# Performance work log

Measured on AMD Instinct MI355X. Metric: run time of the kernel, lower is better.

## Reference

```python
import jax, jax.numpy as jnp
import numpy as np

EPS = 1e-5

def setup_inputs() -> dict:
    key = jax.random.key(0)
    k1, k2, k3 = jax.random.split(key, 3)
    B, T, D, K = 8, 4096, 256, 2048
    x = jax.random.normal(k1, (B, T, D), dtype=jnp.float32)
    embedding_sum = jax.random.normal(k2, (K, D), dtype=jnp.float32)
    cluster_usage = jax.random.uniform(k3, (K,), dtype=jnp.float32)
    return {"x": x, "embedding_sum": embedding_sum, "cluster_usage": cluster_usage}

def reference(x, embedding_sum, cluster_usage):
    # embedding = embedding_sum / clamp(cluster_usage, eps)  -> [K, D]
    emb = embedding_sum / jnp.clip(cluster_usage, EPS, None)[:, None]
    shape = x.shape
    flat = x.reshape(-1, shape[-1])  # [N, D]
    # squared Euclidean distances (argmin-equivalent to torch.cdist p=2)
    d = (
        jnp.sum(flat * flat, axis=-1, keepdims=True)
        - 2.0 * flat @ emb.T
        + jnp.sum(emb * emb, axis=-1)
    )  # [N, K]
    flat_codes = jnp.argmin(d, axis=-1)  # [N]
    codes = flat_codes.reshape(shape[:-1])  # [B, T]
    quantized = emb[codes]  # [B, T, D]
    return quantized, codes
```

## Files before the change

kernel.cpp:

```cpp
#include <hip/hip_runtime.h>


#define EPSV 1e-5f
#define TAU  0.4f
#define DDIM 256
#define BM   128
#define BCL  128
#define NPART 2
#define NCT  8
#define RPB  8
#define KSPL 4
#define NROWS 32768
#define EB   32

typedef __attribute__((ext_vector_type(8))) _Float16 f16x8;
typedef __attribute__((ext_vector_type(4))) float f32x4;
typedef unsigned short u16;
typedef unsigned u32;
typedef unsigned long long u64;

__device__ __forceinline__ u16 f2h(float f) {
    f = fminf(fmaxf(f, -60000.f), 60000.f);
    const _Float16 h = (_Float16)f;
    return __builtin_bit_cast(u16, h);
}
__device__ __forceinline__ u32 umn(u32 a, u32 b) { return a < b ? a : b; }
__device__ __forceinline__ u32 umx(u32 a, u32 b) { return a > b ? a : b; }
__device__ __forceinline__ float unsort(u32 u) {
    const u32 v = (u & 0x80000000u) ? (u & 0x7FFFFFFFu) : ~u;
    return __builtin_bit_cast(float, v);
}
__device__ __forceinline__ u64 packdk(float d, int k) {
    u32 u = __builtin_bit_cast(u32, d);
    u = (u & 0x80000000u) ? ~u : (u | 0x80000000u);
    return ((u64)u << 32) | (u32)k;
}

__global__ void prep(const float* __restrict__ esum,
                     const float* __restrict__ usage,
                     const float* __restrict__ x,
                     float* __restrict__ emb_t,
                     u16* __restrict__ eh,
                     float* __restrict__ enorm2,
                     u16* __restrict__ xh,
                     int* __restrict__ counter,
                     int K) {
    const int b = blockIdx.x;
    const int NEB = K / EB;
    if (b == 0 && threadIdx.x == 0) *counter = 0;
    if (b < NEB) {
        __shared__ float tile[EB][DDIM + 1];
        const int k0 = b * EB;
        const int d  = threadIdx.x;
        for (int r = 0; r < EB; ++r) {
            const int k = k0 + r;
            const float u = fmaxf(usage[k], EPSV);
            const float e = esum[(size_t)k * DDIM + d] / u;
            tile[r][d] = e;
            eh[(size_t)k * DDIM + d] = f2h(e);
        }
        __syncthreads();
        if (threadIdx.x < EB) {
            const int r = threadIdx.x;
            float s = 0.f;
            #pragma unroll 8
            for (int dd = 0; dd < DDIM; ++dd) {
                const float e = tile[r][dd];
                s = fmaf(e, e, s);
            }
            enorm2[k0 + r] = s;
        }
        for (int it = 0; it < DDIM / 8; ++it) {
            const int dd   = it * 8 + (threadIdx.x >> 5);
            const int lane = threadIdx.x & 31;
            emb_t[(size_t)dd * K + k0 + lane] = tile[lane][dd];
        }
    } else {
        const int n = (b - NEB) * 4 + (threadIdx.x >> 6);
        const int l = threadIdx.x & 63;
        const float4 v = *(const float4*)&x[(size_t)n * DDIM + l * 4];
        ushort4 h;
        h.x = f2h(v.x); h.y = f2h(v.y); h.z = f2h(v.z); h.w = f2h(v.w);
        *(ushort4*)&xh[(size_t)n * DDIM + l * 4] = h;
    }
}

__global__ __launch_bounds__(256, 2) void vq_mfma(
        const u16* __restrict__ xh, const u16* __restrict__ eh,
        const float* __restrict__ enorm2,
        u32* __restrict__ pp1, u32* __restrict__ pp2, int N) {
    __shared__ __align__(16) u16 Als[BM * 64];
    __shared__ __align__(16) u16 Bls[BCL * 64];

    const int tid = threadIdx.x;
    const int l   = tid & 63;
    const int w   = tid >> 6;
    const int wr  = w >> 1, wc = w & 1;

    const int nwg = (N / BM) * NPART;
    const int q   = nwg >> 3;
    const int pb  = blockIdx.x;
    const int logical = (pb & 7) * q + (pb >> 3);
    const int rowblk  = logical >> 1;
    const int part    = logical & 1;
    const int n0      = rowblk * BM;
    const int cbase   = part * 1024;

    u32 m1p[4][4], m2p[4][4];
    #pragma unroll
    for (int a = 0; a < 4; ++a)
        #pragma unroll
        for (int b = 0; b < 4; ++b) { m1p[a][b] = 0xFFFFFFFFu; m2p[a][b] = 0xFFFFFFFFu; }

    const int sgc = (l & 7) ^ ((l >> 3) & 7);

    for (int ct = 0; ct < NCT; ++ct) {
        const int c0 = cbase + ct * BCL;
        f32x4 acc[4][4];
        #pragma unroll
        for (int a = 0; a < 4; ++a)
            #pragma unroll
            for (int b = 0; b < 4; ++b) acc[a][b] = (f32x4){0.f, 0.f, 0.f, 0.f};

        for (int ch = 0; ch < 4; ++ch) {
            const int colof = ch * 64;

            __syncthreads();
            #pragma unroll
            for (int j = 0; j < 4; ++j) {
                const int r = (w * 4 + j) * 8 + (l >> 3);
                const u16* ga = xh + (size_t)(n0 + r) * DDIM + colof + sgc * 8;
                __builtin_amdgcn_global_load_lds(
                    (const __attribute__((address_space(1))) void*)ga,
                    (__attribute__((address_space(3))) void*)((char*)Als + (w * 4 + j) * 1024),
                    16, 0, 0);
            }
            #pragma unroll
            for (int j = 0; j < 4; ++j) {
                const int r = (w * 4 + j) * 8 + (l >> 3);
                const u16* gb = eh + (size_t)(c0 + r) * DDIM + colof + sgc * 8;
                __builtin_amdgcn_global_load_lds(
                    (const __attribute__((address_space(1))) void*)gb,
                    (__attribute__((address_space(3))) void*)((char*)Bls + (w * 4 + j) * 1024),
                    16, 0, 0);
            }
            __syncthreads();

            #pragma unroll
            for (int ks = 0; ks < 2; ++ks) {
                f16x8 af[4], bfr[4];
                #pragma unroll
                for (int f = 0; f < 4; ++f) {
                    const int arow = wr * 64 + f * 16 + (l & 15);
                    const int ac   = (ks * 4 + (l >> 4)) ^ (l & 7);
                    af[f] = *(const f16x8*)((const char*)Als + arow * 128 + ac * 16);
                    const int brow = wc * 64 + f * 16 + (l & 15);
                    const int bc   = (ks * 4 + (l >> 4)) ^ (l & 7);
                    bfr[f] = *(const f16x8*)((const char*)Bls + brow * 128 + bc * 16);
                }
                #pragma unroll
                for (int fm = 0; fm < 4; ++fm)
                    #pragma unroll
                    for (int fn = 0; fn < 4; ++fn)
                        acc[fm][fn] = __builtin_amdgcn_mfma_f32_16x16x32_f16(
                            af[fm], bfr[fn], acc[fm][fn], 0, 0, 0);
            }
        }

        #pragma unroll
        for (int fn = 0; fn < 4; ++fn) {
            const int k = c0 + wc * 64 + fn * 16 + (l & 15);
            const float en = enorm2[k];
            #pragma unroll
            for (int fm = 0; fm < 4; ++fm)
                #pragma unroll
                for (int i = 0; i < 4; ++i) {
                    const float s = fmaf(-2.0f, acc[fm][fn][i], en);
                    u32 u = __builtin_bit_cast(u32, s);
                    u = ((int)u < 0) ? ~u : (u | 0x80000000u);
                    const u32 p = (u & 0xFFFFF800u) | (u32)k;
                    m2p[fm][i] = umn(m2p[fm][i], umx(p, m1p[fm][i]));
                    m1p[fm][i] = umn(m1p[fm][i], p);
                }
        }
    }

    #pragma unroll
    for (int fm = 0; fm < 4; ++fm)
        #pragma unroll
        for (int i = 0; i < 4; ++i) {
            u32 p1 = m1p[fm][i], p2 = m2p[fm][i];
            #pragma unroll
            for (int mask = 1; mask < 16; mask <<= 1) {
                const u32 o1 = (u32)__shfl_xor((int)p1, mask, 64);
                const u32 o2 = (u32)__shfl_xor((int)p2, mask, 64);
                p2 = umn(umn(p2, o2), umx(p1, o1));
                p1 = umn(p1, o1);
            }
            m1p[fm][i] = p1; m2p[fm][i] = p2;
        }

    __syncthreads();
    u32* S1 = (u32*)Als;
    u32* S2 = (u32*)((char*)Als + 512);
    if (wc == 0 && (l & 15) == 0) {
        #pragma unroll
        for (int fm = 0; fm < 4; ++fm)
            #pragma unroll
            for (int i = 0; i < 4; ++i) {
                const int r = wr * 64 + fm * 16 + (l >> 4) * 4 + i;
                S1[r] = m1p[fm][i]; S2[r] = m2p[fm][i];
            }
    }
    __syncthreads();
    if (wc == 1 && (l & 15) == 0) {
        #pragma unroll
        for (int fm = 0; fm < 4; ++fm)
            #pragma unroll
            for (int i = 0; i < 4; ++i) {
                const int r = wr * 64 + fm * 16 + (l >> 4) * 4 + i;
                const u32 o1 = S1[r], o2 = S2[r];
                u32 p1 = m1p[fm][i], p2 = m2p[fm][i];
                const u32 M2 = umn(umn(p2, o2), umx(p1, o1));
                const u32 M1 = umn(p1, o1);
                const int n = n0 + r;
                pp1[(size_t)part * N + n] = M1;
                pp2[(size_t)part * N + n] = M2;
            }
    }
}

__global__ void combine(const u32* __restrict__ pp1, const u32* __restrict__ pp2,
                        int* __restrict__ codes_i, int* __restrict__ flags,
                        int* __restrict__ list, int* __restrict__ counter,
                        u64* __restrict__ packed, int N) {
    const int n = blockIdx.x * 256 + threadIdx.x;
    u32 p1 = pp1[n], p2 = pp2[n];
    #pragma unroll
    for (int j = 1; j < NPART; ++j) {
        const u32 o1 = pp1[(size_t)j * N + n], o2 = pp2[(size_t)j * N + n];
        p2 = umn(umn(p2, o2), umx(p1, o1));
        p1 = umn(p1, o1);
    }
    codes_i[n] = (int)(p1 & 0x7FFu);
    const float m1f = unsort(p1 & 0xFFFFF800u);
    const float m2f = unsort(p2 & 0xFFFFF800u);
    const int fl = (m2f - m1f < TAU) ? 1 : 0;
    flags[n] = fl;
    if (fl) {
        packed[n] = 0xFFFFFFFFFFFFFFFFull;
        const int idx = atomicAdd(counter, 1);
        list[idx] = n;
    }
}

__global__ __launch_bounds__(256) void rescue_c(
        const float* __restrict__ x, const float* __restrict__ emb_t,
        const float* __restrict__ enorm2,
        const int* __restrict__ list, const int* __restrict__ counter,
        u64* __restrict__ packed, int K) {
    __shared__ float xs[RPB][DDIM];
    const int t = threadIdx.x;
    const int l = t & 63;
    int cnt = *counter;
    cnt = cnt < 0 ? 0 : (cnt > NROWS ? NROWS : cnt);
    if (cnt == 0) return;
    const int nblk  = (cnt + RPB - 1) / RPB;
    const int items = nblk * KSPL;
    const int kc    = K / KSPL;

    for (int wi = blockIdx.x; wi < items; wi += gridDim.x) {
        const int g = wi >> 2;
        const int q = wi & 3;
        const int base = g * RPB;
        int rows[RPB];
        #pragma unroll
        for (int r = 0; r < RPB; ++r) {
            int idx = base + r;
            rows[r] = list[idx < cnt ? idx : cnt - 1];
        }
        __syncthreads();
        #pragma unroll
        for (int r = 0; r < RPB; ++r)
            xs[r][t] = x[(size_t)rows[r] * DDIM + t];
        __syncthreads();

        float acc[RPB][2];
        #pragma unroll
        for (int r = 0; r < RPB; ++r) { acc[r][0] = 0.f; acc[r][1] = 0.f; }

        const float* eb = emb_t + q * kc + 2 * t;
        #pragma unroll 4
        for (int d = 0; d < DDIM; ++d) {
            const float2 e = *(const float2*)&eb[(size_t)d * K];
            #pragma unroll
            for (int r = 0; r < RPB; ++r) {
                const float xv = xs[r][d];
                acc[r][0] = fmaf(xv, e.x, acc[r][0]);
                acc[r][1] = fmaf(xv, e.y, acc[r][1]);
            }
        }

        const int k0 = q * kc + 2 * t;
        const float en0 = enorm2[k0], en1 = enorm2[k0 + 1];
        #pragma unroll
        for (int r = 0; r < RPB; ++r) {
            const float s0 = fmaf(-2.0f, acc[r][0], en0);
            const float s1 = fmaf(-2.0f, acc[r][1], en1);
            float bd = s0; int bk = k0;
            if (s1 < bd) { bd = s1; bk = k0 + 1; }
            #pragma unroll
            for (int m = 1; m < 64; m <<= 1) {
                const float od = __shfl_xor(bd, m, 64);
                const int   ok = __shfl_xor(bk, m, 64);
                if (od < bd || (od == bd && ok < bk)) { bd = od; bk = ok; }
            }
            if (l == 0) atomicMin(&packed[rows[r]], packdk(bd, bk));
        }
    }
}

__global__ void gather_q(const float* __restrict__ esum,
                         const float* __restrict__ usage,
                         const int* __restrict__ codes_i,
                         const int* __restrict__ flags,
                         const u64* __restrict__ packed,
                         float* __restrict__ qout,
                         float* __restrict__ codes_f) {
    const int n = blockIdx.x * 4 + (threadIdx.x >> 6);
    const int c = threadIdx.x & 63;
    int k = codes_i[n];
    if (flags[n]) k = (int)(packed[n] & 0xFFFFFFFFull);
    if (c == 0) codes_f[n] = (float)k;
    const float u = fmaxf(usage[k], EPSV);
    float4 v = *(const float4*)&esum[(size_t)k * DDIM + c * 4];
    v.x /= u; v.y /= u; v.z /= u; v.w /= u;
    *(float4*)&qout[(size_t)n * DDIM + c * 4] = v;
}

extern "C" void kernel_launch(void* const* d_in, const int* in_sizes, int n_in,
                              void* d_out, int out_size, void* d_ws, size_t ws_size,
                              hipStream_t stream) {
    const float* x     = (const float*)d_in[0];
    const float* esum  = (const float*)d_in[1];
    const float* usage = (const float*)d_in[2];
    const int K = in_sizes[2];
    const int N = in_sizes[0] / DDIM;

    char* p = (char*)d_ws;
    u64*   packed  = (u64*)p;                  p += (size_t)N * 8;
    float* emb_t   = (float*)p;                p += (size_t)K * DDIM * 4;
    float* enorm2  = (float*)p;                p += (size_t)K * 4;
    u32*   pp1     = (u32*)p;                  p += (size_t)NPART * N * 4;
    u32*   pp2     = (u32*)p;                  p += (size_t)NPART * N * 4;
    int*   codes_i = (int*)p;                  p += (size_t)N * 4;
    int*   flags   = (int*)p;                  p += (size_t)N * 4;
    int*   list    = (int*)p;                  p += (size_t)N * 4;
    int*   counter = (int*)p;                  p += 256;
    u16*   xh      = (u16*)p;                  p += (size_t)N * DDIM * 2;
    u16*   eh      = (u16*)p;                  p += (size_t)K * DDIM * 2;

    float* qout    = (float*)d_out;
    float* codes_f = qout + (size_t)N * DDIM;

    prep<<<K / EB + N / 4, 256, 0, stream>>>(esum, usage, x, emb_t, eh,
                                             enorm2, xh, counter, K);
    vq_mfma<<<(N / BM) * NPART, 256, 0, stream>>>(xh, eh, enorm2, pp1, pp2, N);
    combine<<<N / 256, 256, 0, stream>>>(pp1, pp2, codes_i, flags,
                                         list, counter, packed, N);
    rescue_c<<<1024, 256, 0, stream>>>(x, emb_t, enorm2, list, counter, packed, K);
    gather_q<<<N / 4, 256, 0, stream>>>(esum, usage, codes_i, flags, packed,
                                        qout, codes_f);
}
```

Measured before the change: 114.8 us.

## Halve row tile to 64 and split codebook columns across four waves

Shrinks the row block from 128 to 64, so each of the four waves now covers all 64 rows and its own 32-column slice of the 128-entry codebook tile. Accumulators per wave drop from 16 to 8 fragments, and launch bounds rise to four workgroups per SM to raise occupancy. The final cross-wave top-2 reduction becomes a four-way merge through shared memory, and global-to-LDS loads are reindexed by linear slot. In exchange, codebook tiles are reloaded twice as often relative to the rows processed, which lowers arithmetic intensity.

```diff
diff --git a/kernel.cpp b/kernel.cpp
--- a/kernel.cpp
+++ b/kernel.cpp
@@ -4,7 +4,7 @@
 #define EPSV 1e-5f
 #define TAU  0.4f
 #define DDIM 256
-#define BM   128
+#define BM   64
 #define BCL  128
 #define NPART 2
 #define NCT  8
@@ -85,7 +85,7 @@
     }
 }
 
-__global__ __launch_bounds__(256, 2) void vq_mfma(
+__global__ __launch_bounds__(256, 4) void vq_mfma(
         const u16* __restrict__ xh, const u16* __restrict__ eh,
         const float* __restrict__ enorm2,
         u32* __restrict__ pp1, u32* __restrict__ pp2, int N) {
@@ -95,7 +95,6 @@
     const int tid = threadIdx.x;
     const int l   = tid & 63;
     const int w   = tid >> 6;
-    const int wr  = w >> 1, wc = w & 1;
 
     const int nwg = (N / BM) * NPART;
     const int q   = nwg >> 3;
@@ -112,64 +111,67 @@
         #pragma unroll
         for (int b = 0; b < 4; ++b) { m1p[a][b] = 0xFFFFFFFFu; m2p[a][b] = 0xFFFFFFFFu; }
 
-    const int sgc = (l & 7) ^ ((l >> 3) & 7);
-
     for (int ct = 0; ct < NCT; ++ct) {
         const int c0 = cbase + ct * BCL;
-        f32x4 acc[4][4];
-        #pragma unroll
-        for (int a = 0; a < 4; ++a)
-            #pragma unroll
-            for (int b = 0; b < 4; ++b) acc[a][b] = (f32x4){0.f, 0.f, 0.f, 0.f};
+        f32x4 acc[4][2];
+        #pragma unroll
+        for (int a = 0; a < 4; ++a) { acc[a][0] = (f32x4){0,0,0,0}; acc[a][1] = (f32x4){0,0,0,0}; }
 
         for (int ch = 0; ch < 4; ++ch) {
             const int colof = ch * 64;
 
             __syncthreads();
             #pragma unroll
+            for (int j = 0; j < 2; ++j) {
+                const int slot = j * 256 + tid;
+                const int row  = slot >> 3;
+                const int gc   = (slot & 7) ^ (row & 7);
+                __builtin_amdgcn_global_load_lds(
+                    (const __attribute__((address_space(1))) void*)
+                        (xh + (size_t)(n0 + row) * DDIM + colof + gc * 8),
+                    (__attribute__((address_space(3))) void*)((char*)Als + slot * 16),
+                    16, 0, 0);
+            }
+            #pragma unroll
             for (int j = 0; j < 4; ++j) {
-                const int r = (w * 4 + j) * 8 + (l >> 3);
-                const u16* ga = xh + (size_t)(n0 + r) * DDIM + colof + sgc * 8;
+                const int slot = j * 256 + tid;
+                const int row  = slot >> 3;
+                const int gc   = (slot & 7) ^ (row & 7);
                 __builtin_amdgcn_global_load_lds(
-                    (const __attribute__((address_space(1))) void*)ga,
-                    (__attribute__((address_space(3))) void*)((char*)Als + (w * 4 + j) * 1024),
+                    (const __attribute__((address_space(1))) void*)
+                        (eh + (size_t)(c0 + row) * DDIM + colof + gc * 8),
+                    (__attribute__((address_space(3))) void*)((char*)Bls + slot * 16),
                     16, 0, 0);
             }
-            #pragma unroll
-            for (int j = 0; j < 4; ++j) {
-                const int r = (w * 4 + j) * 8 + (l >> 3);
-                const u16* gb = eh + (size_t)(c0 + r) * DDIM + colof + sgc * 8;
-                __builtin_amdgcn_global_load_lds(
-                    (const __attribute__((address_space(1))) void*)gb,
-                    (__attribute__((address_space(3))) void*)((char*)Bls + (w * 4 + j) * 1024),
-                    16, 0, 0);
-            }
             __syncthreads();
 
             #pragma unroll
             for (int ks = 0; ks < 2; ++ks) {
-                f16x8 af[4], bfr[4];
+                f16x8 af[4], bfr[2];
                 #pragma unroll
                 for (int f = 0; f < 4; ++f) {
-                    const int arow = wr * 64 + f * 16 + (l & 15);
+                    const int arow = f * 16 + (l & 15);
                     const int ac   = (ks * 4 + (l >> 4)) ^ (l & 7);
                     af[f] = *(const f16x8*)((const char*)Als + arow * 128 + ac * 16);
-                    const int brow = wc * 64 + f * 16 + (l & 15);
+                }
+                #pragma unroll
+                for (int f = 0; f < 2; ++f) {
+                    const int brow = w * 32 + f * 16 + (l & 15);
                     const int bc   = (ks * 4 + (l >> 4)) ^ (l & 7);
                     bfr[f] = *(const f16x8*)((const char*)Bls + brow * 128 + bc * 16);
                 }
                 #pragma unroll
                 for (int fm = 0; fm < 4; ++fm)
                     #pragma unroll
-                    for (int fn = 0; fn < 4; ++fn)
+                    for (int fn = 0; fn < 2; ++fn)
                         acc[fm][fn] = __builtin_amdgcn_mfma_f32_16x16x32_f16(
                             af[fm], bfr[fn], acc[fm][fn], 0, 0, 0);
             }
         }
 
         #pragma unroll
-        for (int fn = 0; fn < 4; ++fn) {
-            const int k = c0 + wc * 64 + fn * 16 + (l & 15);
+        for (int fn = 0; fn < 2; ++fn) {
+            const int k = c0 + w * 32 + fn * 16 + (l & 15);
             const float en = enorm2[k];
             #pragma unroll
             for (int fm = 0; fm < 4; ++fm)
@@ -202,31 +204,29 @@
 
     __syncthreads();
     u32* S1 = (u32*)Als;
-    u32* S2 = (u32*)((char*)Als + 512);
-    if (wc == 0 && (l & 15) == 0) {
+    u32* S2 = (u32*)((char*)Als + 1024);
+    if ((l & 15) == 0) {
         #pragma unroll
         for (int fm = 0; fm < 4; ++fm)
             #pragma unroll
             for (int i = 0; i < 4; ++i) {
-                const int r = wr * 64 + fm * 16 + (l >> 4) * 4 + i;
-                S1[r] = m1p[fm][i]; S2[r] = m2p[fm][i];
+                const int r = fm * 16 + (l >> 4) * 4 + i;
+                S1[w * 64 + r] = m1p[fm][i];
+                S2[w * 64 + r] = m2p[fm][i];
             }
     }
     __syncthreads();
-    if (wc == 1 && (l & 15) == 0) {
-        #pragma unroll
-        for (int fm = 0; fm < 4; ++fm)
-            #pragma unroll
-            for (int i = 0; i < 4; ++i) {
-                const int r = wr * 64 + fm * 16 + (l >> 4) * 4 + i;
-                const u32 o1 = S1[r], o2 = S2[r];
-                u32 p1 = m1p[fm][i], p2 = m2p[fm][i];
-                const u32 M2 = umn(umn(p2, o2), umx(p1, o1));
-                const u32 M1 = umn(p1, o1);
-                const int n = n0 + r;
-                pp1[(size_t)part * N + n] = M1;
-                pp2[(size_t)part * N + n] = M2;
-            }
+    if (tid < BM) {
+        u32 p1 = S1[tid], p2 = S2[tid];
+        #pragma unroll
+        for (int j = 1; j < 4; ++j) {
+            const u32 o1 = S1[j * 64 + tid], o2 = S2[j * 64 + tid];
+            p2 = umn(umn(p2, o2), umx(p1, o1));
+            p1 = umn(p1, o1);
+        }
+        const int n = n0 + tid;
+        pp1[(size_t)part * N + n] = p1;
+        pp2[(size_t)part * N + n] = p2;
     }
 }
 
```

After: 121.2 us. 1.06x slower.
